# Kernel optimization log

Hardware: AMD Instinct MI355X
Metric: run time of the kernel (lower is better)

The kernel has to match this reference:

```python
import jax, jax.numpy as jnp
import numpy as np

EPSILON = 0.01        # temperature
DIST_THRESH = 0.2
NUM_ITERS = 8         # sparse_rebalance_iters (== num_iters here)
TOPK = 64             # topk_support
NEG_INF = -1e9


def setup_inputs() -> dict:
    key = jax.random.key(0)
    k1, k2, k3 = jax.random.split(key, 3)
    B, N, M, D = 4, 4096, 4096, 128
    return {
        "source_feats": jax.random.normal(k1, (B, N, D), dtype=jnp.float32),
        "source_locs": jax.random.uniform(k2, (B, N, 2), dtype=jnp.float32),
        "target_locs": jax.random.uniform(k3, (B, M, 2), dtype=jnp.float32),
        "source_valid_mask": jnp.ones((B, N), dtype=bool),
        "target_valid_mask": jnp.ones((B, M), dtype=bool),
    }


def _sinkhorn_attn(source_locs, target_locs, source_valid_mask, target_valid_mask):
    # pairwise squared distances: [B, M, N]
    diff = target_locs[:, :, None, :] - source_locs[:, None, :, :]
    dist_sq = jnp.sum(diff * diff, axis=-1)
    log_k = -dist_sq / (EPSILON + 1e-8)
    valid = (dist_sq < DIST_THRESH ** 2)
    valid = valid & source_valid_mask[:, None, :] & target_valid_mask[:, :, None]

    B, M, N = valid.shape
    topk = min(TOPK, N)
    if topk < N:
        masked_log_k = jnp.where(valid, log_k, NEG_INF)
        _, topk_idx = jax.lax.top_k(masked_log_k, topk)  # [B, M, topk]
        support = jnp.zeros_like(valid).at[
            jnp.arange(B)[:, None, None], jnp.arange(M)[None, :, None], topk_idx
        ].set(True)
        valid = valid & support

    log_k = jnp.where(valid, log_k, NEG_INF)

    v = jnp.zeros((B, 1, N), dtype=log_k.dtype)
    u = jnp.zeros((B, M, 1), dtype=log_k.dtype)
    for _ in range(NUM_ITERS):
        u = -jax.nn.logsumexp(log_k + v, axis=2, keepdims=True)
        v = -jax.nn.logsumexp(log_k + u, axis=1, keepdims=True)
        v = jnp.where(source_valid_mask[:, None, :], v, 0.0)

    attn = jnp.exp(log_k + u + v)              # [B, M, N]
    has_source = valid.any(axis=-1, keepdims=True)  # [B, M, 1]
    return attn, has_source


def reference(source_feats, source_locs, target_locs, source_valid_mask, target_valid_mask):
    attn, has_source = _sinkhorn_attn(source_locs, target_locs,
                                      source_valid_mask, target_valid_mask)
    target_feats = jnp.einsum('bmn,bnd->bmd', attn, source_feats)
    target_feats = target_feats * target_valid_mask[:, :, None].astype(target_feats.dtype)
    target_feats = target_feats * has_source.astype(target_feats.dtype)
    return target_feats
```

## Files before the change

### kernel.cpp

```cpp
#include <hip/hip_runtime.h>
#include <math.h>

#define B 4
#define N 4096
#define M 4096
#define D 128
#define K 64
#define BT 256
#define WPB 4
#define RPW 4
#define CAP 640
#define CUTCAP 64
#define PC 128
#define SCAP 1280
#define EPS_DENOM 0.01000001f
#define THRESH2 0.04f
#define GC 16

__device__ __forceinline__ unsigned bf16hi(float f){
    unsigned u = __float_as_uint(f);
    return (u + 0x7FFFu + ((u >> 16) & 1u)) & 0xFFFF0000u;
}

__global__ __launch_bounds__(1024) void k_sort(const float* __restrict__ slocs,
        const float* __restrict__ tlocs,
        float4* __restrict__ sPack, float4* __restrict__ tPack,
        int* __restrict__ cellStart,
        int* __restrict__ colcnt, int* __restrict__ E, int* __restrict__ R,
        float* __restrict__ extraF, float* __restrict__ ics){
    __shared__ int hist[256], startS[256], fill[256], wtot[4];
    __shared__ float2 loc[N];
    __shared__ unsigned short scell[N];
    const int blk = blockIdx.x, tid = threadIdx.x;
    const bool tgt = blk >= B;
    const int b = tgt ? (blk - B) : blk;
    const int lane = tid & 63, w = tid >> 6;
    const float2* slp = (const float2*)((tgt ? tlocs : slocs) + (size_t)b * N * 2);
    float4* outPack = (tgt ? tPack : sPack) + (size_t)b * N;

    if (!tgt){
        for (int i = tid; i < N; i += 1024){
            colcnt[b * N + i] = 0;
            ics[b * N + i] = 1.0f;
        }
        if (b == 0){
            if (tid < B){ E[tid] = 0; R[tid] = 0; }
            if (tid < B * D) extraF[tid] = 0.f;
        }
    }

    if (tid < 256){ hist[tid] = 0; fill[tid] = 0; }
    __syncthreads();
    for (int i = tid; i < N; i += 1024){
        float2 p = slp[i];
        int cx = min(GC - 1, max(0, (int)(p.x * (float)GC)));
        int cy = min(GC - 1, max(0, (int)(p.y * (float)GC)));
        int cell = cy * GC + cx;
        loc[i] = p; scell[i] = (unsigned short)cell;
        atomicAdd(&hist[cell], 1);
    }
    __syncthreads();
    int hv = (tid < 256) ? hist[tid] : 0;
    int pre = hv;
    #pragma unroll
    for (int o = 1; o < 64; o <<= 1){ int t2 = __shfl_up(pre, o, 64); if (lane >= o) pre += t2; }
    if (tid < 256 && lane == 63) wtot[w] = pre;
    __syncthreads();
    if (tid < 256){
        int off = 0;
        for (int i = 0; i < w; ++i) off += wtot[i];
        int st = off + pre - hv;
        startS[tid] = st;
        if (!tgt) cellStart[b * 257 + tid] = st;
    }
    if (!tgt && tid == 0) cellStart[b * 257 + 256] = N;
    __syncthreads();
    for (int i = tid; i < N; i += 1024){
        int cell = scell[i];
        int pos = startS[cell] + atomicAdd(&fill[cell], 1);
        float2 p = loc[i];
        outPack[pos] = make_float4(p.x, p.y, __int_as_float(i), 0.f);
    }
}

__global__ __launch_bounds__(BT, 6) void k_build(const float4* __restrict__ sPack,
        const int* __restrict__ cellStart, const float4* __restrict__ tPack,
        unsigned* __restrict__ csrP, int* __restrict__ cnt,
        int* __restrict__ colcnt, unsigned* __restrict__ cscP,
        int* __restrict__ R){
    __shared__ int cs[257];
    __shared__ float2 sxy[SCAP];
    __shared__ int    sid[SCAP];
    __shared__ unsigned short cj[WPB][CAP];
    __shared__ int   hist[WPB][64];
    __shared__ float cutd[WPB][CUTCAP];
    __shared__ int   cutn[WPB][CUTCAP];
    __shared__ float4 rowT[16];
    __shared__ int gB[16], gL[16], lB[16];
    __shared__ int stot;

    const int bid  = blockIdx.x;
    const int sb   = (bid & 7) * 128 + (bid >> 3);
    const int b    = sb >> 8;
    const int s00  = (sb & 255) * (WPB * RPW);
    const int tid  = threadIdx.x;
    const int w    = tid >> 6;
    const int lane = tid & 63;
    const unsigned long long pmask = (lane == 0) ? 0ull : ((1ull << lane) - 1);
    const float4* sp = sPack + (size_t)b * N;
    const float4* tp = tPack + (size_t)b * M;

    for (int i = tid; i < 257; i += BT) cs[i] = cellStart[b * 257 + i];
    if (tid < 16) rowT[tid] = tp[s00 + tid];
    __syncthreads();

    float txmin = 1e9f, txmax = -1e9f, tymin = 1e9f, tymax = -1e9f;
    #pragma unroll
    for (int i = 0; i < 16; ++i){
        float4 t = rowT[i];
        txmin = fminf(txmin, t.x); txmax = fmaxf(txmax, t.x);
        tymin = fminf(tymin, t.y); tymax = fmaxf(tymax, t.y);
    }
    const int bcy0 = max(0, (int)floorf((tymin - 0.2f) * (float)GC - 0.001f));
    const int bcy1 = min(GC - 1, (int)floorf((tymax + 0.2f) * (float)GC + 0.001f));
    const int ncy  = bcy1 - bcy0 + 1;
    if (tid < ncy && tid < 16){
        int cy = bcy0 + tid;
        float rowLo = cy * 0.0625f, rowHi = rowLo + 0.0625f;
        float dymin = fmaxf(0.f, fmaxf(rowLo - tymax, tymin - rowHi));
        float dxm = sqrtf(fmaxf(THRESH2 - dymin * dymin + 1e-5f, 0.f));
        int cx0 = max(0, (int)floorf((txmin - dxm) * (float)GC - 0.001f));
        int cx1 = min(GC - 1, (int)floorf((txmax + dxm) * (float)GC + 0.001f));
        int s = cs[cy * GC + cx0], e = cs[cy * GC + cx1 + 1];
        gB[tid] = s; gL[tid] = e - s;
    }
    __syncthreads();
    if (tid == 0){
        if (ncy > 16) stot = SCAP + 1;
        else {
            int acc = 0;
            for (int i = 0; i < ncy; ++i){ lB[i] = acc; acc += gL[i]; }
            stot = acc;
        }
    }
    __syncthreads();
    const bool staged = (stot <= SCAP);
    if (staged){
        for (int i = 0; i < ncy; ++i){
            int s = gB[i], len = gL[i], l0 = lB[i];
            for (int j = tid; j < len; j += BT){
                float4 q = sp[s + j];
                sxy[l0 + j] = make_float2(q.x, q.y);
                sid[l0 + j] = ((s + j) << 16) | __float_as_int(q.z);
            }
        }
    }
    __syncthreads();

    for (int r = 0; r < RPW; ++r){
        const int srt   = s00 + w * RPW + r;
        const int srid  = b * M + srt;
        const float4 t  = rowT[w * RPW + r];
        const float tx  = t.x;
        const float ty  = t.y;

        hist[w][lane] = 0;

        const int cy0 = max(0, (int)floorf((ty - 0.2f) * (float)GC - 0.001f));
        const int cy1 = min(GC - 1, (int)floorf((ty + 0.2f) * (float)GC + 0.001f));

        int c = 0;
        for (int cy = cy0; cy <= cy1; ++cy){
            float rowLo = cy * 0.0625f, rowHi = rowLo + 0.0625f;
            float dymin = fmaxf(0.f, fmaxf(rowLo - ty, ty - rowHi));
            float dxm = sqrtf(fmaxf(THRESH2 - dymin * dymin + 1e-5f, 0.f));
            int cx0 = max(0, (int)floorf((tx - dxm) * (float)GC - 0.001f));
            int cx1 = min(GC - 1, (int)floorf((tx + dxm) * (float)GC + 0.001f));
            int s = cs[cy * GC + cx0], e = cs[cy * GC + cx1 + 1];
            int len = e - s;
            int base_l = staged ? (lB[cy - bcy0] + (s - gB[cy - bcy0])) : s;
            for (int j0 = 0; j0 < len; j0 += 64){
                int i = j0 + lane;
                bool valid = i < len;
                int lp = base_l + i;
                float d2 = 1e9f;
                if (valid){
                    float qx, qy;
                    if (staged){ float2 q = sxy[lp]; qx = q.x; qy = q.y; }
                    else       { float4 q = sp[lp];  qx = q.x; qy = q.y; }
                    float dx = __fsub_rn(tx, qx);
                    float dy = __fsub_rn(ty, qy);
                    d2 = __fadd_rn(__fmul_rn(dx, dx), __fmul_rn(dy, dy));
                }
                bool in = valid && (d2 < THRESH2);
                unsigned long long ml = __ballot(in);
                if (in){
                    int p = c + __popcll(ml & pmask);
                    if (p < CAP) cj[w][p] = (unsigned short)lp;
                    atomicAdd(&hist[w][min((int)(d2 * 1600.0f), 63)], 1);
                }
                c += __popcll(ml);
            }
        }
        const int ctot = min(c, CAP);

        int h = hist[w][lane];
        int pre = h;
        #pragma unroll
        for (int o = 1; o < 64; o <<= 1){
            int t2 = __shfl_up(pre, o, 64);
            if (lane >= o) pre += t2;
        }
        int cutB = 64, q = 0;
        if (c > K){
            unsigned long long ge = __ballot(pre >= K);
            int fb = __ffsll((long long)ge) - 1;
            cutB = fb;
            q = K - __shfl(pre - h, fb, 64);
        }

        int base = 0, cutc = 0;
        for (int i0 = 0; i0 < ctot; i0 += 64){
            int i = i0 + lane;
            bool valid = i < ctot;
            float d2 = 1e9f; int pk = 0;
            if (valid){
                int lp = cj[w][i];
                float qx, qy;
                if (staged){ float2 q = sxy[lp]; qx = q.x; qy = q.y; pk = sid[lp]; }
                else       { float4 q = sp[lp];  qx = q.x; qy = q.y;
                             pk = (lp << 16) | __float_as_int(q.z); }
                float dx = __fsub_rn(tx, qx);
                float dy = __fsub_rn(ty, qy);
                d2 = __fadd_rn(__fmul_rn(dx, dx), __fmul_rn(dy, dy));
            }
            int bk = valid ? min((int)(d2 * 1600.0f), 63) : 64;
            bool low = valid && (bk < cutB);
            unsigned long long ml = __ballot(low);
            if (low){
                int p = base + __popcll(ml & pmask);
                unsigned eb = bf16hi(expf(-(d2 / EPS_DENOM)));
                int cpos = pk >> 16;
                csrP[(size_t)srid * K + p] = eb | (unsigned)cpos;
                int bn = (b << 12) + cpos;
                int slot = atomicAdd(&colcnt[bn], 1);
                if (slot < PC)
                    cscP[(size_t)bn * PC + slot] = eb | (unsigned)srt;
            }
            base += __popcll(ml);
            if (cutB < 64){
                bool eq = valid && (bk == cutB);
                unsigned long long me = __ballot(eq);
                if (eq){
                    int p = cutc + __popcll(me & pmask);
                    if (p < CUTCAP){ cutd[w][p] = d2; cutn[w][p] = pk; }
                }
                cutc += __popcll(me);
            }
        }

        if (c > K){
            int cc = min(cutc, CUTCAP);
            {
                int i = lane;
                bool sel = false; float d2i = 0.f; int ni = 0;
                if (i < cc){
                    d2i = cutd[w][i]; ni = cutn[w][i];
                    int rank = 0;
                    for (int j = 0; j < cc; ++j){
                        float dj = cutd[w][j]; int nj = cutn[w][j];
                        rank += (dj < d2i) || (dj == d2i && (nj & 0xFFFF) < (ni & 0xFFFF));
                    }
                    sel = rank < q;
                }
                unsigned long long ms = __ballot(sel);
                if (sel){
                    int p = base + __popcll(ms & pmask);
                    unsigned eb = bf16hi(expf(-(d2i / EPS_DENOM)));
                    int cpos = ni >> 16;
                    csrP[(size_t)srid * K + p] = eb | (unsigned)cpos;
                    int bn = (b << 12) + cpos;
                    int slot = atomicAdd(&colcnt[bn], 1);
                    if (slot < PC)
                        cscP[(size_t)bn * PC + slot] = eb | (unsigned)srt;
                }
            }
            if (lane == 0) cnt[srid] = K;
        } else {
            if (lane == 0){
                cnt[srid] = c;
                if (c == 0) atomicAdd(&R[b], 1);
            }
        }
    }
}

__global__ __launch_bounds__(256) void k_prep(const int* __restrict__ colcnt,
        int* __restrict__ E, const float* __restrict__ feats,
        const float4* __restrict__ sPack, float* __restrict__ extraF){
    int t = blockIdx.x * blockDim.x + threadIdx.x;
    int lane = t & 63, b = t >> 12;
    int cc = colcnt[t];
    unsigned long long em = __ballot(cc == 0);
    if (lane == 0 && em) atomicAdd(&E[b], __popcll(em));
    if (cc == 0){
        int orig = __float_as_int(sPack[t].z);
        for (int d = 0; d < D; ++d)
            atomicAdd(&extraF[b * D + d], feats[((size_t)((b << 12) + orig)) * D + d]);
    }
}

__global__ __launch_bounds__(256) void kA(const unsigned* __restrict__ csrP,
        const int* __restrict__ cnt,
        const float* __restrict__ ics, const int* __restrict__ E,
        float* __restrict__ eu, int first){
    int t = blockIdx.x * blockDim.x + threadIdx.x;
    int W = t >> 6, lane = t & 63;
    for (int rr = 0; rr < 4; ++rr){
        int rid = W * 4 + rr;
        int b = rid >> 12;
        int c = cnt[rid];
        float s = 0.f;
        if (lane < c){
            unsigned pe = csrP[(size_t)rid * K + lane];
            float e = __uint_as_float(pe & 0xFFFF0000u);
            s = first ? e : e * ics[(b << 12) + (pe & 0xFFFFu)];
        }
        #pragma unroll
        for (int o = 32; o; o >>= 1) s += __shfl_xor(s, o, 64);
        int Eb = E[b];
        if (c == 0 && Eb == 0){
            if (lane == 0) eu[rid] = 0.f;
        } else {
            if (Eb > 0) s += (float)Eb;
            if (lane == 0) eu[rid] = 1.0f / s;
        }
    }
}

__global__ __launch_bounds__(256) void kB(const unsigned* __restrict__ cscP,
        const int* __restrict__ colcnt,
        const float* __restrict__ eu, const int* __restrict__ R, float* __restrict__ ics){
    int t = blockIdx.x * blockDim.x + threadIdx.x;
    int W = t >> 6, lane = t & 63;
    for (int rr = 0; rr < 4; ++rr){
        int cid = W * 4 + rr;
        int b = cid >> 12;
        int cc = min(colcnt[cid], PC);
        float s = 0.f;
        for (int p = lane; p < cc; p += 64){
            unsigned pe = cscP[(size_t)cid * PC + p];
            s += __uint_as_float(pe & 0xFFFF0000u) * eu[(b << 12) + (pe & 0xFFFFu)];
        }
        #pragma unroll
        for (int o = 32; o; o >>= 1) s += __shfl_xor(s, o, 64);
        if (lane == 0)
            ics[cid] = 1.0f / (s + (float)R[b]);
    }
}

__global__ __launch_bounds__(128) void k_out(const float* __restrict__ feats,
        const unsigned* __restrict__ csrP,
        const int* __restrict__ cnt, const float* __restrict__ eu,
        const float* __restrict__ ics, const float* __restrict__ extraF,
        const float4* __restrict__ sPack, const float4* __restrict__ tPack,
        float* __restrict__ out){
    __shared__ float att[K];
    __shared__ int   sidx[K];
    int bid = blockIdx.x;
    int sg  = (bid & 7) * 2048 + (bid >> 3);
    int b   = sg >> 12;
    int srt = sg & 4095;
    int m   = __float_as_int(tPack[(size_t)b * M + srt].z);
    const float4* sp = sPack + (size_t)b * N;
    int tid = threadIdx.x;
    int c = cnt[sg];
    if (tid < K){
        float a = 0.f; int ix = 0;
        if (tid < c){
            unsigned pe = csrP[(size_t)sg * K + tid];
            int cpos = pe & 0xFFFFu;
            a = __uint_as_float(pe & 0xFFFF0000u) * eu[sg] * ics[(b << 12) + cpos];
            ix = __float_as_int(sp[cpos].z);
        }
        att[tid] = a; sidx[tid] = ix;
    }
    __syncthreads();
    float acc = 0.f;
    if (c > 0){
        acc = extraF[b * D + tid];
        for (int k = 0; k < c; ++k)
            acc += att[k] * feats[((size_t)((b << 12) + sidx[k])) * D + tid];
    }
    out[((size_t)((b << 12) + m)) * D + tid] = acc;
}

extern "C" void kernel_launch(void* const* d_in, const int* in_sizes, int n_in,
                              void* d_out, int out_size, void* d_ws, size_t ws_size,
                              hipStream_t stream){
    const float* feats = (const float*)d_in[0];
    const float* slocs = (const float*)d_in[1];
    const float* tlocs = (const float*)d_in[2];
    float* out = (float*)d_out;

    char* w = (char*)d_ws;
    size_t off = 0;
    auto carve = [&](size_t bytes) -> void* {
        void* p = w + off;
        off += (bytes + 255) & ~(size_t)255;
        return p;
    };
    unsigned* csrP  = (unsigned*)carve((size_t)B * M * K * 4);
    unsigned* cscP  = (unsigned*)carve((size_t)B * N * PC * 4);
    int*   cnt     = (int*)  carve((size_t)B * M * 4);
    int*   colcnt  = (int*)  carve((size_t)B * N * 4);
    float* eu      = (float*)carve((size_t)B * M * 4);
    float* ics     = (float*)carve((size_t)B * N * 4);
    int*   E       = (int*)  carve(B * 4);
    int*   R       = (int*)  carve(B * 4);
    float* extraF  = (float*)carve((size_t)B * D * 4);
    float4* sPack  = (float4*)carve((size_t)B * N * 16);
    float4* tPack  = (float4*)carve((size_t)B * M * 16);
    int*   cellStart = (int*)carve((size_t)B * 257 * 4);

    k_sort<<<2 * B, 1024, 0, stream>>>(slocs, tlocs, sPack, tPack, cellStart,
                                       colcnt, E, R, extraF, ics);
    k_build<<<B * M / (WPB * RPW), BT, 0, stream>>>(sPack, cellStart, tPack,
            csrP, cnt, colcnt, cscP, R);
    k_prep<<<(B * N) / 256, 256, 0, stream>>>(colcnt, E, feats, sPack, extraF);
    for (int it = 0; it < 8; ++it){
        kA<<<B * M / 16, 256, 0, stream>>>(csrP, cnt, ics, E, eu, it == 0 ? 1 : 0);
        kB<<<B * N / 16, 256, 0, stream>>>(cscP, colcnt, eu, R, ics);
    }
    k_out<<<B * M, D, 0, stream>>>(feats, csrP, cnt, eu, ics, extraF, sPack, tPack, out);
}
```

Before: 252.1 us.

## Precompute row sums in build to skip first row pass, one row per wave

k_build now accumulates each row's kernel-value sum while emitting CSR entries and stores it in a new rs array. The first Sinkhorn column pass derives eu on the fly from rs, which removes one kA launch. kA and kB now handle one row or column per wave with four times as many blocks, instead of looping over four per wave. It also raises the staging and cut capacities, lets the cut-selection loop run over two 64-wide chunks, and lowers k_build's occupancy hint from 6 to 5. This trades extra shared memory and lower occupancy in k_build for fewer launches and more parallelism in the iteration kernels.

```diff
diff --git a/kernel.cpp b/kernel.cpp
--- a/kernel.cpp
+++ b/kernel.cpp
@@ -9,10 +9,10 @@
 #define BT 256
 #define WPB 4
 #define RPW 4
-#define CAP 640
-#define CUTCAP 64
+#define CAP 768
+#define CUTCAP 128
 #define PC 128
-#define SCAP 1280
+#define SCAP 1536
 #define EPS_DENOM 0.01000001f
 #define THRESH2 0.04f
 #define GC 16
@@ -83,11 +83,11 @@
     }
 }
 
-__global__ __launch_bounds__(BT, 6) void k_build(const float4* __restrict__ sPack,
+__global__ __launch_bounds__(BT, 5) void k_build(const float4* __restrict__ sPack,
         const int* __restrict__ cellStart, const float4* __restrict__ tPack,
         unsigned* __restrict__ csrP, int* __restrict__ cnt,
         int* __restrict__ colcnt, unsigned* __restrict__ cscP,
-        int* __restrict__ R){
+        int* __restrict__ R, float* __restrict__ rs){
     __shared__ int cs[257];
     __shared__ float2 sxy[SCAP];
     __shared__ int    sid[SCAP];
@@ -165,6 +165,7 @@
         const float ty  = t.y;
 
         hist[w][lane] = 0;
+        float rsum = 0.f;
 
         const int cy0 = max(0, (int)floorf((ty - 0.2f) * (float)GC - 0.001f));
         const int cy1 = min(GC - 1, (int)floorf((ty + 0.2f) * (float)GC + 0.001f));
@@ -240,6 +241,7 @@
             if (low){
                 int p = base + __popcll(ml & pmask);
                 unsigned eb = bf16hi(expf(-(d2 / EPS_DENOM)));
+                rsum += __uint_as_float(eb);
                 int cpos = pk >> 16;
                 csrP[(size_t)srid * K + p] = eb | (unsigned)cpos;
                 int bn = (b << 12) + cpos;
@@ -261,8 +263,8 @@
 
         if (c > K){
             int cc = min(cutc, CUTCAP);
-            {
-                int i = lane;
+            for (int i0 = 0; i0 < CUTCAP; i0 += 64){
+                int i = i0 + lane;
                 bool sel = false; float d2i = 0.f; int ni = 0;
                 if (i < cc){
                     d2i = cutd[w][i]; ni = cutn[w][i];
@@ -277,6 +279,7 @@
                 if (sel){
                     int p = base + __popcll(ms & pmask);
                     unsigned eb = bf16hi(expf(-(d2i / EPS_DENOM)));
+                    rsum += __uint_as_float(eb);
                     int cpos = ni >> 16;
                     csrP[(size_t)srid * K + p] = eb | (unsigned)cpos;
                     int bn = (b << 12) + cpos;
@@ -284,6 +287,8 @@
                     if (slot < PC)
                         cscP[(size_t)bn * PC + slot] = eb | (unsigned)srt;
                 }
+                base += __popcll(ms);
+                if (i0 + 64 >= cc) break;
             }
             if (lane == 0) cnt[srid] = K;
         } else {
@@ -292,6 +297,9 @@
                 if (c == 0) atomicAdd(&R[b], 1);
             }
         }
+        #pragma unroll
+        for (int o = 32; o; o >>= 1) rsum += __shfl_xor(rsum, o, 64);
+        if (lane == 0) rs[srid] = rsum;
     }
 }
 
@@ -313,50 +321,54 @@
 __global__ __launch_bounds__(256) void kA(const unsigned* __restrict__ csrP,
         const int* __restrict__ cnt,
         const float* __restrict__ ics, const int* __restrict__ E,
-        float* __restrict__ eu, int first){
+        float* __restrict__ eu){
     int t = blockIdx.x * blockDim.x + threadIdx.x;
-    int W = t >> 6, lane = t & 63;
-    for (int rr = 0; rr < 4; ++rr){
-        int rid = W * 4 + rr;
-        int b = rid >> 12;
-        int c = cnt[rid];
-        float s = 0.f;
-        if (lane < c){
-            unsigned pe = csrP[(size_t)rid * K + lane];
-            float e = __uint_as_float(pe & 0xFFFF0000u);
-            s = first ? e : e * ics[(b << 12) + (pe & 0xFFFFu)];
-        }
-        #pragma unroll
-        for (int o = 32; o; o >>= 1) s += __shfl_xor(s, o, 64);
-        int Eb = E[b];
-        if (c == 0 && Eb == 0){
-            if (lane == 0) eu[rid] = 0.f;
-        } else {
-            if (Eb > 0) s += (float)Eb;
-            if (lane == 0) eu[rid] = 1.0f / s;
-        }
+    int rid = t >> 6, lane = t & 63;
+    int b = rid >> 12;
+    int c = cnt[rid];
+    float s = 0.f;
+    if (lane < c){
+        unsigned pe = csrP[(size_t)rid * K + lane];
+        s = __uint_as_float(pe & 0xFFFF0000u) * ics[(b << 12) + (pe & 0xFFFFu)];
+    }
+    #pragma unroll
+    for (int o = 32; o; o >>= 1) s += __shfl_xor(s, o, 64);
+    int Eb = E[b];
+    if (c == 0 && Eb == 0){
+        if (lane == 0) eu[rid] = 0.f;
+    } else {
+        if (Eb > 0) s += (float)Eb;
+        if (lane == 0) eu[rid] = 1.0f / s;
     }
 }
 
 __global__ __launch_bounds__(256) void kB(const unsigned* __restrict__ cscP,
         const int* __restrict__ colcnt,
-        const float* __restrict__ eu, const int* __restrict__ R, float* __restrict__ ics){
+        const float* __restrict__ eu, const int* __restrict__ R,
+        float* __restrict__ ics,
+        const float* __restrict__ rs, const int* __restrict__ E, int first){
     int t = blockIdx.x * blockDim.x + threadIdx.x;
-    int W = t >> 6, lane = t & 63;
-    for (int rr = 0; rr < 4; ++rr){
-        int cid = W * 4 + rr;
-        int b = cid >> 12;
-        int cc = min(colcnt[cid], PC);
-        float s = 0.f;
+    int cid = t >> 6, lane = t & 63;
+    int b = cid >> 12;
+    int cc = min(colcnt[cid], PC);
+    float s = 0.f;
+    if (first){
+        float Eb = (float)E[b];
+        for (int p = lane; p < cc; p += 64){
+            unsigned pe = cscP[(size_t)cid * PC + p];
+            float euv = 1.0f / (rs[(b << 12) + (pe & 0xFFFFu)] + Eb);
+            s += __uint_as_float(pe & 0xFFFF0000u) * euv;
+        }
+    } else {
         for (int p = lane; p < cc; p += 64){
             unsigned pe = cscP[(size_t)cid * PC + p];
             s += __uint_as_float(pe & 0xFFFF0000u) * eu[(b << 12) + (pe & 0xFFFFu)];
         }
-        #pragma unroll
-        for (int o = 32; o; o >>= 1) s += __shfl_xor(s, o, 64);
-        if (lane == 0)
-            ics[cid] = 1.0f / (s + (float)R[b]);
-    }
+    }
+    #pragma unroll
+    for (int o = 32; o; o >>= 1) s += __shfl_xor(s, o, 64);
+    if (lane == 0)
+        ics[cid] = 1.0f / (s + (float)R[b]);
 }
 
 __global__ __launch_bounds__(128) void k_out(const float* __restrict__ feats,
@@ -416,6 +428,7 @@
     int*   colcnt  = (int*)  carve((size_t)B * N * 4);
     float* eu      = (float*)carve((size_t)B * M * 4);
     float* ics     = (float*)carve((size_t)B * N * 4);
+    float* rs      = (float*)carve((size_t)B * M * 4);
     int*   E       = (int*)  carve(B * 4);
     int*   R       = (int*)  carve(B * 4);
     float* extraF  = (float*)carve((size_t)B * D * 4);
@@ -426,11 +439,13 @@
     k_sort<<<2 * B, 1024, 0, stream>>>(slocs, tlocs, sPack, tPack, cellStart,
                                        colcnt, E, R, extraF, ics);
     k_build<<<B * M / (WPB * RPW), BT, 0, stream>>>(sPack, cellStart, tPack,
-            csrP, cnt, colcnt, cscP, R);
+            csrP, cnt, colcnt, cscP, R, rs);
     k_prep<<<(B * N) / 256, 256, 0, stream>>>(colcnt, E, feats, sPack, extraF);
-    for (int it = 0; it < 8; ++it){
-        kA<<<B * M / 16, 256, 0, stream>>>(csrP, cnt, ics, E, eu, it == 0 ? 1 : 0);
-        kB<<<B * N / 16, 256, 0, stream>>>(cscP, colcnt, eu, R, ics);
+
+    kB<<<B * N / 4, 256, 0, stream>>>(cscP, colcnt, eu, R, ics, rs, E, 1);
+    for (int it = 1; it < 8; ++it){
+        kA<<<B * M / 4, 256, 0, stream>>>(csrP, cnt, ics, E, eu);
+        kB<<<B * N / 4, 256, 0, stream>>>(cscP, colcnt, eu, R, ics, rs, E, 0);
     }
     k_out<<<B * M, D, 0, stream>>>(feats, csrP, cnt, eu, ics, extraF, sPack, tPack, out);
 }
```

Result: faster. 232.2 us (median of 2 runs) (-7.9%).
